# Performance work log

Measured on AMD Instinct MI355X. Metric: run time of the kernel, lower is better.

The kernel has to match this reference:

```python
import jax, jax.numpy as jnp
import numpy as np

D_EMBED = 1024
D_MODEL = 1024
NUM_HEADS = 16
DEPTH = D_MODEL // NUM_HEADS


def setup_inputs() -> dict:
    key = jax.random.key(0)
    ks = jax.random.split(key, 11)
    B, S = 2, 2048
    s = 0.02
    return {
        "query": jax.random.normal(ks[0], (B, S, D_EMBED), jnp.float32),
        "key": jax.random.normal(ks[1], (B, S, D_EMBED), jnp.float32),
        "value": jax.random.normal(ks[2], (B, S, D_EMBED), jnp.float32),
        "wq": jax.random.normal(ks[3], (D_EMBED, D_MODEL), jnp.float32) * s,
        "bq": jnp.zeros((D_MODEL,), jnp.float32),
        "wk": jax.random.normal(ks[4], (D_EMBED, D_MODEL), jnp.float32) * s,
        "bk": jnp.zeros((D_MODEL,), jnp.float32),
        "wv": jax.random.normal(ks[5], (D_EMBED, D_MODEL), jnp.float32) * s,
        "bv": jnp.zeros((D_MODEL,), jnp.float32),
        "wf": jax.random.normal(ks[6], (D_MODEL, D_MODEL), jnp.float32) * s,
        "bf": jnp.zeros((D_MODEL,), jnp.float32),
    }


def _split_heads(x, B):
    # [B, S, d_model] -> [B, H, S, depth]
    S = x.shape[1]
    return x.reshape(B, S, NUM_HEADS, DEPTH).transpose(0, 2, 1, 3)


def reference(query, key, value, wq, bq, wk, bk, wv, bv, wf, bf):
    B = query.shape[0]
    q = _split_heads(query @ wq + bq, B)
    k = _split_heads(key @ wk + bk, B)
    v = _split_heads(value @ wv + bv, B)
    # NOTE: source calls calculate_attention(query, key, value) against a
    # signature (value, key, query) -> scores use V_proj, output contracts Q_proj.
    scores = jnp.einsum("bhsd,bhtd->bhst", v, k) / np.sqrt(DEPTH).astype(np.float32)
    probs = jax.nn.softmax(scores, axis=-1)  # [B, H, S, S]
    attn = jnp.einsum("bhst,bhtd->bhsd", probs, q)
    out = attn.transpose(0, 2, 1, 3).reshape(B, -1, D_MODEL)
    out = out @ wf + bf
    return out, probs
```

## Files before the change

kernel.cpp:

```cpp
#include <hip/hip_runtime.h>
#include <hip/hip_bf16.h>
#include <math.h>


typedef float f32x4 __attribute__((ext_vector_type(4)));
typedef __bf16 bf16x8 __attribute__((ext_vector_type(8)));
typedef __bf16 bf16x4 __attribute__((ext_vector_type(4)));

#define LOG2E 1.44269504088896340736f

static __device__ __forceinline__ f32x4 mfma16x16x32(bf16x8 a, bf16x8 b, f32x4 c) {
    return __builtin_amdgcn_mfma_f32_16x16x32_bf16(a, b, c, 0, 0, 0);
}

__global__ void __launch_bounds__(256) wtrans_kernel(
    const float* __restrict__ w0, const float* __restrict__ w1,
    const float* __restrict__ w2, const float* __restrict__ w3,
    __bf16* __restrict__ o0, __bf16* __restrict__ o1,
    __bf16* __restrict__ o2, __bf16* __restrict__ o3)
{
    const float* W; __bf16* O;
    switch (blockIdx.z) {
        case 0: W = w0; O = o0; break;
        case 1: W = w1; O = o1; break;
        case 2: W = w2; O = o2; break;
        default: W = w3; O = o3; break;
    }
    __shared__ float tile[32][33];
    int tx = threadIdx.x, ty = threadIdx.y;
    int n0 = blockIdx.x * 32, k0 = blockIdx.y * 32;
    #pragma unroll
    for (int j = 0; j < 32; j += 8)
        tile[ty + j][tx] = W[(size_t)(k0 + ty + j) * 1024 + n0 + tx];
    __syncthreads();
    #pragma unroll
    for (int j = 0; j < 32; j += 8)
        O[(size_t)(n0 + ty + j) * 1024 + k0 + tx] = (__bf16)tile[tx][ty + j];
}

__global__ void __launch_bounds__(256) proj_gemm(
    const float* __restrict__ X, const __bf16* __restrict__ Wt,
    const float* __restrict__ bias, __bf16* __restrict__ outN,
    __bf16* __restrict__ outQt)
{
    int lane = threadIdx.x & 63, wid = threadIdx.x >> 6;
    int g = lane >> 4, sl = lane & 15;
    int bm0 = blockIdx.y * 64, bn0 = blockIdx.x * 64;
    int arow = bm0 + wid * 16 + sl;

    f32x4 acc[4] = {};
    const float* ap = X + (size_t)arow * 1024 + g * 8;
    const __bf16* bp0 = Wt + (size_t)(bn0 + sl) * 1024 + g * 8;

    for (int kk = 0; kk < 32; ++kk) {
        f32x4 x0 = *(const f32x4*)(ap);
        f32x4 x1 = *(const f32x4*)(ap + 4);
        ap += 32;
        bf16x8 a;
        a[0]=(__bf16)x0[0]; a[1]=(__bf16)x0[1]; a[2]=(__bf16)x0[2]; a[3]=(__bf16)x0[3];
        a[4]=(__bf16)x1[0]; a[5]=(__bf16)x1[1]; a[6]=(__bf16)x1[2]; a[7]=(__bf16)x1[3];
        #pragma unroll
        for (int nt = 0; nt < 4; ++nt) {
            bf16x8 b = *(const bf16x8*)(bp0 + (size_t)nt * 16 * 1024 + kk * 32);
            acc[nt] = mfma16x16x32(a, b, acc[nt]);
        }
    }
    #pragma unroll
    for (int nt = 0; nt < 4; ++nt) {
        int n = bn0 + nt * 16 + sl;
        float bv = bias[n];
        #pragma unroll
        for (int r = 0; r < 4; ++r) {
            int mrow = bm0 + wid * 16 + g * 4 + r;
            float vv = acc[nt][r] + bv;
            if (outQt) {
                int b = mrow >> 11, s = mrow & 2047;
                int h = n >> 6, d = n & 63;
                outQt[((size_t)((b * 16 + h) * 64 + d)) * 2048 + s] = (__bf16)vv;
            } else {
                outN[(size_t)mrow * 1024 + n] = (__bf16)vv;
            }
        }
    }
}

__global__ void __launch_bounds__(256) flash_attn(
    const __bf16* __restrict__ Qt, const __bf16* __restrict__ Kp,
    const __bf16* __restrict__ Vp, float* __restrict__ probs,
    __bf16* __restrict__ attn)
{
    __shared__ __bf16 pl[4][16][40];
    int lane = threadIdx.x & 63, wid = threadIdx.x >> 6;
    int g = lane >> 4, sl = lane & 15;
    int bh = blockIdx.y, b = bh >> 4, h = bh & 15;
    int s0 = blockIdx.x * 64 + wid * 16;

    const __bf16* kbase  = Kp + (size_t)b * 2048 * 1024 + h * 64;
    const __bf16* vbase  = Vp + (size_t)b * 2048 * 1024 + h * 64;
    const __bf16* qtbase = Qt + (size_t)bh * 64 * 2048;

    const __bf16* vp = vbase + (size_t)(s0 + sl) * 1024 + g * 8;
    bf16x8 vlo = *(const bf16x8*)(vp);
    bf16x8 vhi = *(const bf16x8*)(vp + 32);

    float m = -INFINITY, lsum = 0.f;
    for (int tt = 0; tt < 128; ++tt) {
        const __bf16* kp = kbase + (size_t)(tt * 16 + sl) * 1024 + g * 8;
        bf16x8 klo = *(const bf16x8*)(kp);
        bf16x8 khi = *(const bf16x8*)(kp + 32);
        f32x4 c = {0.f, 0.f, 0.f, 0.f};
        c = mfma16x16x32(klo, vlo, c);
        c = mfma16x16x32(khi, vhi, c);
        float v0 = c[0]*0.125f, v1 = c[1]*0.125f, v2 = c[2]*0.125f, v3 = c[3]*0.125f;
        float tmax = fmaxf(fmaxf(v0, v1), fmaxf(v2, v3));
        float mn = fmaxf(m, tmax);
        float sum4 = exp2f((v0-mn)*LOG2E) + exp2f((v1-mn)*LOG2E)
                   + exp2f((v2-mn)*LOG2E) + exp2f((v3-mn)*LOG2E);
        lsum = lsum * exp2f((m - mn) * LOG2E) + sum4;
        m = mn;
    }
    #pragma unroll
    for (int off = 16; off < 64; off <<= 1) {
        float mo = __shfl_xor(m, off);
        float lo = __shfl_xor(lsum, off);
        float mn = fmaxf(m, mo);
        lsum = lsum * exp2f((m - mn)*LOG2E) + lo * exp2f((mo - mn)*LOG2E);
        m = mn;
    }
    float inv_l = 1.0f / lsum;

    float* prow = probs + (size_t)bh * 2048 * 2048 + (size_t)(s0 + sl) * 2048;
    __bf16* plrow = &pl[wid][sl][0];
    f32x4 accd[4] = {};
    for (int t2 = 0; t2 < 64; ++t2) {
        const __bf16* kpa = kbase + (size_t)(t2 * 32 + sl) * 1024 + g * 8;
        const __bf16* kpb = kpa + (size_t)16 * 1024;
        bf16x8 kloa = *(const bf16x8*)(kpa);
        bf16x8 khia = *(const bf16x8*)(kpa + 32);
        bf16x8 klob = *(const bf16x8*)(kpb);
        bf16x8 khib = *(const bf16x8*)(kpb + 32);
        f32x4 ca = {0.f,0.f,0.f,0.f}, cb = {0.f,0.f,0.f,0.f};
        ca = mfma16x16x32(kloa, vlo, ca); ca = mfma16x16x32(khia, vhi, ca);
        cb = mfma16x16x32(klob, vlo, cb); cb = mfma16x16x32(khib, vhi, cb);

        f32x4 pa, pb;
        #pragma unroll
        for (int j = 0; j < 4; ++j) {
            pa[j] = exp2f((ca[j]*0.125f - m) * LOG2E) * inv_l;
            pb[j] = exp2f((cb[j]*0.125f - m) * LOG2E) * inv_l;
        }
        *(f32x4*)(prow + t2*32 + g*4)      = pa;
        *(f32x4*)(prow + t2*32 + 16 + g*4) = pb;

        bf16x4 wa, wb;
        wa[0]=(__bf16)pa[0]; wa[1]=(__bf16)pa[1]; wa[2]=(__bf16)pa[2]; wa[3]=(__bf16)pa[3];
        wb[0]=(__bf16)pb[0]; wb[1]=(__bf16)pb[1]; wb[2]=(__bf16)pb[2]; wb[3]=(__bf16)pb[3];
        *(bf16x4*)(plrow + g*4)      = wa;
        *(bf16x4*)(plrow + 16 + g*4) = wb;
        bf16x8 pfrag = *(const bf16x8*)(&pl[wid][sl][g*8]);

        #pragma unroll
        for (int dt = 0; dt < 4; ++dt) {
            bf16x8 qf = *(const bf16x8*)(qtbase + (size_t)(dt*16 + sl) * 2048 + t2*32 + g*8);
            accd[dt] = mfma16x16x32(pfrag, qf, accd[dt]);
        }
    }
    __bf16* abase = attn + ((size_t)(b * 2048 + s0)) * 1024 + h * 64;
    #pragma unroll
    for (int dt = 0; dt < 4; ++dt) {
        #pragma unroll
        for (int r = 0; r < 4; ++r) {
            abase[(size_t)(g*4 + r) * 1024 + dt*16 + sl] = (__bf16)accd[dt][r];
        }
    }
}

__global__ void __launch_bounds__(256) final_gemm(
    const __bf16* __restrict__ A, const __bf16* __restrict__ Wt,
    const float* __restrict__ bias, float* __restrict__ out)
{
    int lane = threadIdx.x & 63, wid = threadIdx.x >> 6;
    int g = lane >> 4, sl = lane & 15;
    int bm0 = blockIdx.y * 64, bn0 = blockIdx.x * 64;
    int arow = bm0 + wid * 16 + sl;

    f32x4 acc[4] = {};
    const __bf16* ap = A + (size_t)arow * 1024 + g * 8;
    const __bf16* bp0 = Wt + (size_t)(bn0 + sl) * 1024 + g * 8;

    for (int kk = 0; kk < 32; ++kk) {
        bf16x8 a = *(const bf16x8*)(ap);
        ap += 32;
        #pragma unroll
        for (int nt = 0; nt < 4; ++nt) {
            bf16x8 b = *(const bf16x8*)(bp0 + (size_t)nt * 16 * 1024 + kk * 32);
            acc[nt] = mfma16x16x32(a, b, acc[nt]);
        }
    }
    #pragma unroll
    for (int nt = 0; nt < 4; ++nt) {
        int n = bn0 + nt * 16 + sl;
        float bv = bias[n];
        #pragma unroll
        for (int r = 0; r < 4; ++r) {
            int mrow = bm0 + wid * 16 + g * 4 + r;
            out[(size_t)mrow * 1024 + n] = acc[nt][r] + bv;
        }
    }
}

extern "C" void kernel_launch(void* const* d_in, const int* in_sizes, int n_in,
                              void* d_out, int out_size, void* d_ws, size_t ws_size,
                              hipStream_t stream)
{
    (void)in_sizes; (void)n_in; (void)out_size; (void)ws_size;
    const float* q  = (const float*)d_in[0];
    const float* k  = (const float*)d_in[1];
    const float* v  = (const float*)d_in[2];
    const float* wq = (const float*)d_in[3];
    const float* bq = (const float*)d_in[4];
    const float* wk = (const float*)d_in[5];
    const float* bk = (const float*)d_in[6];
    const float* wv = (const float*)d_in[7];
    const float* bv = (const float*)d_in[8];
    const float* wf = (const float*)d_in[9];
    const float* bf = (const float*)d_in[10];

    char* ws = (char*)d_ws;
    __bf16* wqT = (__bf16*)(ws);
    __bf16* wkT = (__bf16*)(ws + (2ull<<20));
    __bf16* wvT = (__bf16*)(ws + (4ull<<20));
    __bf16* wfT = (__bf16*)(ws + (6ull<<20));
    __bf16* Qt  = (__bf16*)(ws + (8ull<<20));
    __bf16* Kp  = (__bf16*)(ws + (16ull<<20));
    __bf16* Vp  = (__bf16*)(ws + (24ull<<20));
    __bf16* At  = (__bf16*)(ws + (32ull<<20));

    float* out   = (float*)d_out;
    float* probs = out + (size_t)4096 * 1024;

    wtrans_kernel<<<dim3(32,32,4), dim3(32,8), 0, stream>>>(wq,wk,wv,wf, wqT,wkT,wvT,wfT);
    proj_gemm<<<dim3(16,64), 256, 0, stream>>>(q, wqT, bq, nullptr, Qt);
    proj_gemm<<<dim3(16,64), 256, 0, stream>>>(k, wkT, bk, Kp, nullptr);
    proj_gemm<<<dim3(16,64), 256, 0, stream>>>(v, wvT, bv, Vp, nullptr);
    flash_attn<<<dim3(32,32), 256, 0, stream>>>(Qt, Kp, Vp, probs, At);
    final_gemm<<<dim3(16,64), 256, 0, stream>>>(At, wfT, bf, out);
}
```

Before: 1.228 ms.

## Tile GEMMs through LDS and split attention key range across two waves

Replaces the per-wave direct-global projection and output GEMMs with one templated 128x64 LDS-tiled GEMM in which each wave computes a 64x32 block, so A and B tiles are reused from shared memory. The attention kernel now uses 512 threads: two waves split the key range of each query-row group, merge their softmax statistics and partial outputs through shared memory, and fold the scale into a single exp2 constant. Probability stores become nontemporal, since the large probs matrix is never re-read. The changes add block-wide syncs and extra LDS use, which may limit occupancy.

```diff
diff --git a/kernel.cpp b/kernel.cpp
--- a/kernel.cpp
+++ b/kernel.cpp
@@ -8,6 +8,7 @@
 typedef __bf16 bf16x4 __attribute__((ext_vector_type(4)));
 
 #define LOG2E 1.44269504088896340736f
+#define K1 0.18033688011112042592f
 
 static __device__ __forceinline__ f32x4 mfma16x16x32(bf16x8 a, bf16x8 b, f32x4 c) {
     return __builtin_amdgcn_mfma_f32_16x16x32_bf16(a, b, c, 0, 0, 0);
@@ -38,174 +39,213 @@
         O[(size_t)(n0 + ty + j) * 1024 + k0 + tx] = (__bf16)tile[tx][ty + j];
 }
 
-__global__ void __launch_bounds__(256) proj_gemm(
-    const float* __restrict__ X, const __bf16* __restrict__ Wt,
-    const float* __restrict__ bias, __bf16* __restrict__ outN,
-    __bf16* __restrict__ outQt)
-{
-    int lane = threadIdx.x & 63, wid = threadIdx.x >> 6;
+template<int MODE, int AFMT>
+__global__ void __launch_bounds__(256) bgemm(
+    const float* __restrict__ Af, const __bf16* __restrict__ Ab,
+    const __bf16* __restrict__ Wt, const float* __restrict__ bias,
+    __bf16* __restrict__ obf, float* __restrict__ of)
+{
+    __shared__ __bf16 As[128][72];
+    __shared__ __bf16 Bs[64][72];
+    int tid = threadIdx.x;
+    int lane = tid & 63, wid = tid >> 6;
     int g = lane >> 4, sl = lane & 15;
-    int bm0 = blockIdx.y * 64, bn0 = blockIdx.x * 64;
-    int arow = bm0 + wid * 16 + sl;
-
-    f32x4 acc[4] = {};
-    const float* ap = X + (size_t)arow * 1024 + g * 8;
-    const __bf16* bp0 = Wt + (size_t)(bn0 + sl) * 1024 + g * 8;
-
-    for (int kk = 0; kk < 32; ++kk) {
-        f32x4 x0 = *(const f32x4*)(ap);
-        f32x4 x1 = *(const f32x4*)(ap + 4);
-        ap += 32;
-        bf16x8 a;
-        a[0]=(__bf16)x0[0]; a[1]=(__bf16)x0[1]; a[2]=(__bf16)x0[2]; a[3]=(__bf16)x0[3];
-        a[4]=(__bf16)x1[0]; a[5]=(__bf16)x1[1]; a[6]=(__bf16)x1[2]; a[7]=(__bf16)x1[3];
-        #pragma unroll
-        for (int nt = 0; nt < 4; ++nt) {
-            bf16x8 b = *(const bf16x8*)(bp0 + (size_t)nt * 16 * 1024 + kk * 32);
-            acc[nt] = mfma16x16x32(a, b, acc[nt]);
-        }
-    }
-    #pragma unroll
-    for (int nt = 0; nt < 4; ++nt) {
-        int n = bn0 + nt * 16 + sl;
+    int wr = wid >> 1, wc = wid & 1;
+    int m0 = blockIdx.y * 128, n0 = blockIdx.x * 64;
+
+    int srow = tid >> 3;
+    int scol = (tid & 7) * 8;
+    int frow = tid >> 4;
+    int fcol = (tid & 15) * 4;
+
+    f32x4 acc[4][2] = {};
+
+    for (int kt = 0; kt < 16; ++kt) {
+        int k0 = kt * 64;
+        __syncthreads();
+        if (AFMT == 1) {
+            #pragma unroll
+            for (int p = 0; p < 8; ++p) {
+                int row = p * 16 + frow;
+                f32x4 x = *(const f32x4*)&Af[(size_t)(m0 + row) * 1024 + k0 + fcol];
+                bf16x4 w;
+                w[0] = (__bf16)x[0]; w[1] = (__bf16)x[1];
+                w[2] = (__bf16)x[2]; w[3] = (__bf16)x[3];
+                *(bf16x4*)&As[row][fcol] = w;
+            }
+        } else {
+            #pragma unroll
+            for (int p = 0; p < 4; ++p) {
+                int row = p * 32 + srow;
+                *(bf16x8*)&As[row][scol] =
+                    *(const bf16x8*)&Ab[(size_t)(m0 + row) * 1024 + k0 + scol];
+            }
+        }
+        #pragma unroll
+        for (int p = 0; p < 2; ++p) {
+            int row = p * 32 + srow;
+            *(bf16x8*)&Bs[row][scol] =
+                *(const bf16x8*)&Wt[(size_t)(n0 + row) * 1024 + k0 + scol];
+        }
+        __syncthreads();
+        #pragma unroll
+        for (int kk = 0; kk < 2; ++kk) {
+            bf16x8 af[4], bfr[2];
+            #pragma unroll
+            for (int mt = 0; mt < 4; ++mt)
+                af[mt] = *(const bf16x8*)&As[wr*64 + mt*16 + sl][kk*32 + g*8];
+            #pragma unroll
+            for (int nt = 0; nt < 2; ++nt)
+                bfr[nt] = *(const bf16x8*)&Bs[wc*32 + nt*16 + sl][kk*32 + g*8];
+            #pragma unroll
+            for (int mt = 0; mt < 4; ++mt)
+                #pragma unroll
+                for (int nt = 0; nt < 2; ++nt)
+                    acc[mt][nt] = mfma16x16x32(af[mt], bfr[nt], acc[mt][nt]);
+        }
+    }
+    #pragma unroll
+    for (int nt = 0; nt < 2; ++nt) {
+        int n = n0 + wc*32 + nt*16 + sl;
         float bv = bias[n];
         #pragma unroll
-        for (int r = 0; r < 4; ++r) {
-            int mrow = bm0 + wid * 16 + g * 4 + r;
-            float vv = acc[nt][r] + bv;
-            if (outQt) {
-                int b = mrow >> 11, s = mrow & 2047;
-                int h = n >> 6, d = n & 63;
-                outQt[((size_t)((b * 16 + h) * 64 + d)) * 2048 + s] = (__bf16)vv;
-            } else {
-                outN[(size_t)mrow * 1024 + n] = (__bf16)vv;
+        for (int mt = 0; mt < 4; ++mt) {
+            #pragma unroll
+            for (int r = 0; r < 4; ++r) {
+                int mrow = m0 + wr*64 + mt*16 + g*4 + r;
+                float vv = acc[mt][nt][r] + bv;
+                if (MODE == 1) {
+                    int b = mrow >> 11, s = mrow & 2047;
+                    int hh = n >> 6, d = n & 63;
+                    obf[((size_t)((b*16 + hh)*64 + d))*2048 + s] = (__bf16)vv;
+                } else if (MODE == 0) {
+                    obf[(size_t)mrow*1024 + n] = (__bf16)vv;
+                } else {
+                    of[(size_t)mrow*1024 + n] = vv;
+                }
             }
         }
     }
 }
 
-__global__ void __launch_bounds__(256) flash_attn(
+__global__ void __launch_bounds__(512, 8) flash_attn(
     const __bf16* __restrict__ Qt, const __bf16* __restrict__ Kp,
     const __bf16* __restrict__ Vp, float* __restrict__ probs,
     __bf16* __restrict__ attn)
 {
-    __shared__ __bf16 pl[4][16][40];
+    __shared__ float mlbuf[4][2][2][16];
+    __shared__ float obuf[4][16][68];
+    __shared__ __bf16 pl[8][16][40];
+
     int lane = threadIdx.x & 63, wid = threadIdx.x >> 6;
     int g = lane >> 4, sl = lane & 15;
+    int rg = wid >> 1, half = wid & 1;
     int bh = blockIdx.y, b = bh >> 4, h = bh & 15;
-    int s0 = blockIdx.x * 64 + wid * 16;
-
-    const __bf16* kbase  = Kp + (size_t)b * 2048 * 1024 + h * 64;
-    const __bf16* vbase  = Vp + (size_t)b * 2048 * 1024 + h * 64;
-    const __bf16* qtbase = Qt + (size_t)bh * 64 * 2048;
-
-    const __bf16* vp = vbase + (size_t)(s0 + sl) * 1024 + g * 8;
+    int s0 = blockIdx.x * 64 + rg * 16;
+    int tb = half * 1024;
+
+    const __bf16* khalf  = Kp + (size_t)b * 2048 * 1024 + h * 64 + (size_t)tb * 1024;
+    const __bf16* qtb    = Qt + (size_t)bh * 64 * 2048 + tb;
+
+    const __bf16* vp = Vp + (size_t)b * 2048 * 1024 + h * 64 + (size_t)(s0 + sl) * 1024 + g * 8;
     bf16x8 vlo = *(const bf16x8*)(vp);
     bf16x8 vhi = *(const bf16x8*)(vp + 32);
 
-    float m = -INFINITY, lsum = 0.f;
-    for (int tt = 0; tt < 128; ++tt) {
-        const __bf16* kp = kbase + (size_t)(tt * 16 + sl) * 1024 + g * 8;
+    float mraw = -1e30f, lsum = 0.f;
+    #pragma unroll 2
+    for (int tt = 0; tt < 64; ++tt) {
+        const __bf16* kp = khalf + (size_t)(tt * 16 + sl) * 1024 + g * 8;
         bf16x8 klo = *(const bf16x8*)(kp);
         bf16x8 khi = *(const bf16x8*)(kp + 32);
         f32x4 c = {0.f, 0.f, 0.f, 0.f};
         c = mfma16x16x32(klo, vlo, c);
         c = mfma16x16x32(khi, vhi, c);
-        float v0 = c[0]*0.125f, v1 = c[1]*0.125f, v2 = c[2]*0.125f, v3 = c[3]*0.125f;
-        float tmax = fmaxf(fmaxf(v0, v1), fmaxf(v2, v3));
-        float mn = fmaxf(m, tmax);
-        float sum4 = exp2f((v0-mn)*LOG2E) + exp2f((v1-mn)*LOG2E)
-                   + exp2f((v2-mn)*LOG2E) + exp2f((v3-mn)*LOG2E);
-        lsum = lsum * exp2f((m - mn) * LOG2E) + sum4;
-        m = mn;
+        float tmax = fmaxf(fmaxf(c[0], c[1]), fmaxf(c[2], c[3]));
+        float mn = fmaxf(mraw, tmax);
+        float sc = mn * K1;
+        float s4 = exp2f(c[0]*K1 - sc) + exp2f(c[1]*K1 - sc)
+                 + exp2f(c[2]*K1 - sc) + exp2f(c[3]*K1 - sc);
+        lsum = lsum * exp2f(mraw * K1 - sc) + s4;
+        mraw = mn;
     }
     #pragma unroll
     for (int off = 16; off < 64; off <<= 1) {
-        float mo = __shfl_xor(m, off);
+        float mo = __shfl_xor(mraw, off);
         float lo = __shfl_xor(lsum, off);
-        float mn = fmaxf(m, mo);
-        lsum = lsum * exp2f((m - mn)*LOG2E) + lo * exp2f((mo - mn)*LOG2E);
-        m = mn;
+        float mn = fmaxf(mraw, mo);
+        lsum = lsum * exp2f((mraw - mn) * K1) + lo * exp2f((mo - mn) * K1);
+        mraw = mn;
+    }
+    if (g == 0) { mlbuf[rg][half][0][sl] = mraw; mlbuf[rg][half][1][sl] = lsum; }
+    __syncthreads();
+    {
+        float m0h = mlbuf[rg][0][0][sl], l0 = mlbuf[rg][0][1][sl];
+        float m1h = mlbuf[rg][1][0][sl], l1 = mlbuf[rg][1][1][sl];
+        float mn = fmaxf(m0h, m1h);
+        lsum = l0 * exp2f((m0h - mn) * K1) + l1 * exp2f((m1h - mn) * K1);
+        mraw = mn;
     }
     float inv_l = 1.0f / lsum;
-
-    float* prow = probs + (size_t)bh * 2048 * 2048 + (size_t)(s0 + sl) * 2048;
+    float msc = mraw * K1;
+
+    float* prow = probs + (size_t)bh * 2048 * 2048 + (size_t)(s0 + sl) * 2048 + tb;
     __bf16* plrow = &pl[wid][sl][0];
     f32x4 accd[4] = {};
-    for (int t2 = 0; t2 < 64; ++t2) {
-        const __bf16* kpa = kbase + (size_t)(t2 * 32 + sl) * 1024 + g * 8;
-        const __bf16* kpb = kpa + (size_t)16 * 1024;
-        bf16x8 kloa = *(const bf16x8*)(kpa);
-        bf16x8 khia = *(const bf16x8*)(kpa + 32);
-        bf16x8 klob = *(const bf16x8*)(kpb);
-        bf16x8 khib = *(const bf16x8*)(kpb + 32);
-        f32x4 ca = {0.f,0.f,0.f,0.f}, cb = {0.f,0.f,0.f,0.f};
-        ca = mfma16x16x32(kloa, vlo, ca); ca = mfma16x16x32(khia, vhi, ca);
-        cb = mfma16x16x32(klob, vlo, cb); cb = mfma16x16x32(khib, vhi, cb);
-
-        f32x4 pa, pb;
-        #pragma unroll
-        for (int j = 0; j < 4; ++j) {
-            pa[j] = exp2f((ca[j]*0.125f - m) * LOG2E) * inv_l;
-            pb[j] = exp2f((cb[j]*0.125f - m) * LOG2E) * inv_l;
-        }
-        *(f32x4*)(prow + t2*32 + g*4)      = pa;
-        *(f32x4*)(prow + t2*32 + 16 + g*4) = pb;
-
-        bf16x4 wa, wb;
-        wa[0]=(__bf16)pa[0]; wa[1]=(__bf16)pa[1]; wa[2]=(__bf16)pa[2]; wa[3]=(__bf16)pa[3];
-        wb[0]=(__bf16)pb[0]; wb[1]=(__bf16)pb[1]; wb[2]=(__bf16)pb[2]; wb[3]=(__bf16)pb[3];
-        *(bf16x4*)(plrow + g*4)      = wa;
-        *(bf16x4*)(plrow + 16 + g*4) = wb;
+    for (int t2 = 0; t2 < 32; ++t2) {
+        {
+            const __bf16* kpa = khalf + (size_t)(t2 * 32 + sl) * 1024 + g * 8;
+            bf16x8 klo = *(const bf16x8*)(kpa);
+            bf16x8 khi = *(const bf16x8*)(kpa + 32);
+            f32x4 c = {0.f,0.f,0.f,0.f};
+            c = mfma16x16x32(klo, vlo, c);
+            c = mfma16x16x32(khi, vhi, c);
+            f32x4 pa;
+            #pragma unroll
+            for (int j = 0; j < 4; ++j) pa[j] = exp2f(c[j]*K1 - msc) * inv_l;
+            __builtin_nontemporal_store(pa, (f32x4*)(prow + t2*32 + g*4));
+            bf16x4 wa;
+            wa[0]=(__bf16)pa[0]; wa[1]=(__bf16)pa[1]; wa[2]=(__bf16)pa[2]; wa[3]=(__bf16)pa[3];
+            *(bf16x4*)(plrow + g*4) = wa;
+        }
+        {
+            const __bf16* kpb = khalf + (size_t)(t2 * 32 + 16 + sl) * 1024 + g * 8;
+            bf16x8 klo = *(const bf16x8*)(kpb);
+            bf16x8 khi = *(const bf16x8*)(kpb + 32);
+            f32x4 c = {0.f,0.f,0.f,0.f};
+            c = mfma16x16x32(klo, vlo, c);
+            c = mfma16x16x32(khi, vhi, c);
+            f32x4 pb;
+            #pragma unroll
+            for (int j = 0; j < 4; ++j) pb[j] = exp2f(c[j]*K1 - msc) * inv_l;
+            __builtin_nontemporal_store(pb, (f32x4*)(prow + t2*32 + 16 + g*4));
+            bf16x4 wb;
+            wb[0]=(__bf16)pb[0]; wb[1]=(__bf16)pb[1]; wb[2]=(__bf16)pb[2]; wb[3]=(__bf16)pb[3];
+            *(bf16x4*)(plrow + 16 + g*4) = wb;
+        }
         bf16x8 pfrag = *(const bf16x8*)(&pl[wid][sl][g*8]);
-
         #pragma unroll
         for (int dt = 0; dt < 4; ++dt) {
-            bf16x8 qf = *(const bf16x8*)(qtbase + (size_t)(dt*16 + sl) * 2048 + t2*32 + g*8);
+            bf16x8 qf = *(const bf16x8*)(qtb + (size_t)(dt*16 + sl) * 2048 + t2*32 + g*8);
             accd[dt] = mfma16x16x32(pfrag, qf, accd[dt]);
         }
     }
-    __bf16* abase = attn + ((size_t)(b * 2048 + s0)) * 1024 + h * 64;
-    #pragma unroll
-    for (int dt = 0; dt < 4; ++dt) {
-        #pragma unroll
-        for (int r = 0; r < 4; ++r) {
-            abase[(size_t)(g*4 + r) * 1024 + dt*16 + sl] = (__bf16)accd[dt][r];
-        }
-    }
-}
-
-__global__ void __launch_bounds__(256) final_gemm(
-    const __bf16* __restrict__ A, const __bf16* __restrict__ Wt,
-    const float* __restrict__ bias, float* __restrict__ out)
-{
-    int lane = threadIdx.x & 63, wid = threadIdx.x >> 6;
-    int g = lane >> 4, sl = lane & 15;
-    int bm0 = blockIdx.y * 64, bn0 = blockIdx.x * 64;
-    int arow = bm0 + wid * 16 + sl;
-
-    f32x4 acc[4] = {};
-    const __bf16* ap = A + (size_t)arow * 1024 + g * 8;
-    const __bf16* bp0 = Wt + (size_t)(bn0 + sl) * 1024 + g * 8;
-
-    for (int kk = 0; kk < 32; ++kk) {
-        bf16x8 a = *(const bf16x8*)(ap);
-        ap += 32;
-        #pragma unroll
-        for (int nt = 0; nt < 4; ++nt) {
-            bf16x8 b = *(const bf16x8*)(bp0 + (size_t)nt * 16 * 1024 + kk * 32);
-            acc[nt] = mfma16x16x32(a, b, acc[nt]);
-        }
-    }
-    #pragma unroll
-    for (int nt = 0; nt < 4; ++nt) {
-        int n = bn0 + nt * 16 + sl;
-        float bv = bias[n];
-        #pragma unroll
-        for (int r = 0; r < 4; ++r) {
-            int mrow = bm0 + wid * 16 + g * 4 + r;
-            out[(size_t)mrow * 1024 + n] = acc[nt][r] + bv;
-        }
+
+    if (half == 0) {
+        #pragma unroll
+        for (int dt = 0; dt < 4; ++dt)
+            #pragma unroll
+            for (int r = 0; r < 4; ++r)
+                obuf[rg][g*4 + r][dt*16 + sl] = accd[dt][r];
+    }
+    __syncthreads();
+    if (half == 1) {
+        __bf16* abase = attn + ((size_t)(b * 2048 + s0)) * 1024 + h * 64;
+        #pragma unroll
+        for (int dt = 0; dt < 4; ++dt)
+            #pragma unroll
+            for (int r = 0; r < 4; ++r)
+                abase[(size_t)(g*4 + r) * 1024 + dt*16 + sl] =
+                    (__bf16)(obuf[rg][g*4 + r][dt*16 + sl] + accd[dt][r]);
     }
 }
 
@@ -239,10 +279,11 @@
     float* out   = (float*)d_out;
     float* probs = out + (size_t)4096 * 1024;
 
+    dim3 gg(16, 32);
     wtrans_kernel<<<dim3(32,32,4), dim3(32,8), 0, stream>>>(wq,wk,wv,wf, wqT,wkT,wvT,wfT);
-    proj_gemm<<<dim3(16,64), 256, 0, stream>>>(q, wqT, bq, nullptr, Qt);
-    proj_gemm<<<dim3(16,64), 256, 0, stream>>>(k, wkT, bk, Kp, nullptr);
-    proj_gemm<<<dim3(16,64), 256, 0, stream>>>(v, wvT, bv, Vp, nullptr);
-    flash_attn<<<dim3(32,32), 256, 0, stream>>>(Qt, Kp, Vp, probs, At);
-    final_gemm<<<dim3(16,64), 256, 0, stream>>>(At, wfT, bf, out);
-}
+    bgemm<1,1><<<gg, 256, 0, stream>>>(q, nullptr, wqT, bq, Qt, nullptr);
+    bgemm<0,1><<<gg, 256, 0, stream>>>(k, nullptr, wkT, bk, Kp, nullptr);
+    bgemm<0,1><<<gg, 256, 0, stream>>>(v, nullptr, wvT, bv, Vp, nullptr);
+    flash_attn<<<dim3(32,32), 512, 0, stream>>>(Qt, Kp, Vp, probs, At);
+    bgemm<2,0><<<gg, 256, 0, stream>>>(nullptr, At, wfT, bf, nullptr, out);
+}
```

Result: faster. 1.126 ms (-8.3%).
